# Performance work log

Measured on AMD Instinct MI355X. Metric: run time of the kernel, lower is better.

Reference implementation:

```python
import jax, jax.numpy as jnp
import numpy as np

EPS = 1e-5

def setup_inputs() -> dict:
    key = jax.random.key(0)
    ks = jax.random.split(key, 4)
    n, c, h, w = 4, 256, 64, 64
    attn_chans = 64
    x = jax.random.normal(ks[0], (n, c, h, w), dtype=jnp.float32)
    gamma = jnp.ones((c,), jnp.float32)
    beta = jnp.zeros((c,), jnp.float32)
    qkv_w = jax.random.normal(ks[1], (c, 3 * c), dtype=jnp.float32) / np.sqrt(c)
    proj_w = jax.random.normal(ks[2], (c, c), dtype=jnp.float32) / np.sqrt(c)
    proj_b = jnp.zeros((c,), jnp.float32)
    return {"x": x, "gamma": gamma, "beta": beta, "qkv_w": qkv_w,
            "proj_w": proj_w, "proj_b": proj_b, "attn_chans": attn_chans}


def reference(x, gamma, beta, qkv_w, proj_w, proj_b, attn_chans):
    n, c, h, w = x.shape
    heads = c // attn_chans
    scale = attn_chans ** 0.5
    # BatchNorm2d (training mode: batch statistics, biased variance)
    mean = jnp.mean(x, axis=(0, 2, 3))
    var = jnp.var(x, axis=(0, 2, 3))
    xn = (x - mean[:, None, None]) * jax.lax.rsqrt(var + EPS)[:, None, None]
    xn = xn * gamma[:, None, None] + beta[:, None, None]
    # (n, c, h, w) -> (n, hw, c)
    seq = jnp.transpose(xn.reshape(n, c, h * w), (0, 2, 1))
    qkv = seq @ qkv_w                             # (n, hw, 3c)
    # faithful to torch: view (n, hw, 3c) as (n, heads, hw, 3*attn_chans)
    qkv = qkv.reshape(n, heads, h * w, 3 * attn_chans)
    q, k, v = jnp.split(qkv, 3, axis=-1)          # each (n, heads, hw, d)
    scores = jnp.einsum('nhqd,nhkd->nhqk', q, k) / scale
    attn = jax.nn.softmax(scores, axis=-1)
    o = jnp.einsum('nhqk,nhkd->nhqd', attn, v)    # (n, heads, hw, d)
    o = o.reshape(n, h * w, heads * attn_chans)   # (n, hw, c)
    out = o @ proj_w + proj_b                     # (n, hw, c)
    return jnp.transpose(out, (0, 2, 1)).reshape(n, c, h, w)
```

## Files before the change

kernel.cpp:

```cpp
#include <hip/hip_runtime.h>
#include <stdint.h>

#define NB 4
#define CCH 256
#define HW 4096
#define HEADS 4
#define DH 64
#define SLEN 4096
#define EPSV 1e-5f
#define NEG_INF (-__builtin_inff())
#define QSCALE (0.125f * 1.44269504088896340736f)

typedef unsigned short u16;
typedef __bf16 bf16x8 __attribute__((ext_vector_type(8)));
typedef float f32x4 __attribute__((ext_vector_type(4)));

__device__ __forceinline__ u16 f2bf(float f) {
  union { float f; uint32_t u; } v; v.f = f;
  uint32_t r = v.u + 0x7FFFu + ((v.u >> 16) & 1u);
  return (u16)(r >> 16);
}

__global__ __launch_bounds__(256) void k_pre(
    const float* __restrict__ x, const float* __restrict__ gamma,
    const float* __restrict__ beta, const float* __restrict__ qw,
    const float* __restrict__ pw, float* __restrict__ ab,
    u16* __restrict__ qwb, u16* __restrict__ pwb) {
  int t = threadIdx.x;
  if (blockIdx.x < 256) {
    int ch = blockIdx.x;
    float s = 0.f, ss = 0.f;
    for (int n = 0; n < NB; ++n) {
      const float4* p = (const float4*)(x + ((size_t)(n * CCH + ch)) * HW);
      for (int i = t; i < HW / 4; i += 256) {
        float4 v = p[i];
        s += v.x + v.y + v.z + v.w;
        ss += v.x * v.x + v.y * v.y + v.z * v.z + v.w * v.w;
      }
    }
#pragma unroll
    for (int mm = 32; mm >= 1; mm >>= 1) {
      s += __shfl_down(s, mm);
      ss += __shfl_down(ss, mm);
    }
    __shared__ float ls[4], lss[4];
    if ((t & 63) == 0) { ls[t >> 6] = s; lss[t >> 6] = ss; }
    __syncthreads();
    if (t == 0) {
      float S = 0.f, SS = 0.f;
      for (int i = 0; i < 4; ++i) { S += ls[i]; SS += lss[i]; }
      float inv = 1.0f / (float)(NB * HW);
      float mean = S * inv;
      float var = SS * inv - mean * mean;
      float a = gamma[ch] * rsqrtf(var + EPSV);
      ab[ch] = a;
      ab[CCH + ch] = beta[ch] - mean * a;
    }
  } else {
    const int NQ = CCH * 3 * CCH;
    int i = ((blockIdx.x - 256) * 256 + t) * 8;
    const float* src = (i < NQ) ? (qw + i) : (pw + (i - NQ));
    u16* dst = (i < NQ) ? (qwb + i) : (pwb + (i - NQ));
    float4 v0 = *(const float4*)src;
    float4 v1 = *(const float4*)(src + 4);
    union { u16 u[8]; uint4 v; } o;
    o.u[0] = f2bf(v0.x); o.u[1] = f2bf(v0.y); o.u[2] = f2bf(v0.z); o.u[3] = f2bf(v0.w);
    o.u[4] = f2bf(v1.x); o.u[5] = f2bf(v1.y); o.u[6] = f2bf(v1.z); o.u[7] = f2bf(v1.w);
    *(uint4*)dst = o.v;
  }
}

__global__ __launch_bounds__(256) void k_seq(
    const float* __restrict__ x, const float* __restrict__ ab,
    u16* __restrict__ seq) {
  __shared__ float tile[64][65];
  int pb = blockIdx.x * 64, cb = blockIdx.y * 64, n = blockIdx.z;
  int t = threadIdx.x;
  {
    int cl = t >> 2, pc = (t & 3) * 16;
    float a = ab[cb + cl], b = ab[CCH + cb + cl];
    const float* src = x + ((size_t)(n * CCH + cb + cl)) * HW + pb + pc;
#pragma unroll
    for (int i = 0; i < 4; ++i) {
      float4 v = *(const float4*)(src + i * 4);
      tile[cl][pc + i * 4 + 0] = v.x * a + b;
      tile[cl][pc + i * 4 + 1] = v.y * a + b;
      tile[cl][pc + i * 4 + 2] = v.z * a + b;
      tile[cl][pc + i * 4 + 3] = v.w * a + b;
    }
  }
  __syncthreads();
  {
    int pl = t >> 2, cs = (t & 3) * 16;
    union { u16 u[16]; uint4 v[2]; } tmp;
#pragma unroll
    for (int i = 0; i < 16; ++i) tmp.u[i] = f2bf(tile[cs + i][pl]);
    u16* dst = seq + ((size_t)(n * HW + pb + pl)) * CCH + cb + cs;
    *(uint4*)dst = tmp.v[0];
    *(uint4*)(dst + 8) = tmp.v[1];
  }
}

__global__ __launch_bounds__(256) void k_qkv(
    const u16* __restrict__ seq, const u16* __restrict__ w,
    u16* __restrict__ Q, u16* __restrict__ K, u16* __restrict__ Vt) {
  __shared__ __attribute__((aligned(16))) u16 As[64 * 32];
  __shared__ __attribute__((aligned(16))) u16 Bs[64 * 32];
  int Rb = blockIdx.x * 64, Cb = blockIdx.y * 64;
  int t = threadIdx.x, lane = t & 63, wv = t >> 6;
  int wr = (wv >> 1) * 32, wc = (wv & 1) * 32;
  f32x4 acc[2][2] = {};
  for (int kb = 0; kb < CCH; kb += 32) {
    {
      int r = t >> 2, kc = t & 3;
      uint4 v = *(const uint4*)(seq + ((size_t)(Rb + r)) * CCH + kb + kc * 8);
      *(uint4*)((char*)As + r * 64 + ((kc * 16) ^ ((r & 3) << 4))) = v;
    }
    {
      int k = t >> 3, jc = (t & 7) * 8;
      union { u16 u[8]; uint4 v; } tmp;
      tmp.v = *(const uint4*)(w + ((size_t)(kb + k)) * 768 + Cb + jc);
#pragma unroll
      for (int i2 = 0; i2 < 8; ++i2) {
        int j = jc + i2;
        *(u16*)((char*)Bs + j * 64 + ((k * 2) ^ ((j & 3) << 4))) = tmp.u[i2];
      }
    }
    __syncthreads();
    bf16x8 af[2], bfr[2];
#pragma unroll
    for (int f = 0; f < 2; ++f) {
      int row = wr + f * 16 + (lane & 15);
      af[f] = *(const bf16x8*)((const char*)As + row * 64 +
                               (((lane >> 4) * 16) ^ ((row & 3) << 4)));
      int col = wc + f * 16 + (lane & 15);
      bfr[f] = *(const bf16x8*)((const char*)Bs + col * 64 +
                                (((lane >> 4) * 16) ^ ((col & 3) << 4)));
    }
#pragma unroll
    for (int i2 = 0; i2 < 2; ++i2)
#pragma unroll
      for (int j2 = 0; j2 < 2; ++j2)
        acc[i2][j2] = __builtin_amdgcn_mfma_f32_16x16x32_bf16(af[i2], bfr[j2], acc[i2][j2], 0, 0, 0);
    __syncthreads();
  }
#pragma unroll
  for (int i2 = 0; i2 < 2; ++i2)
#pragma unroll
    for (int j2 = 0; j2 < 2; ++j2)
#pragma unroll
      for (int e = 0; e < 4; ++e) {
        int R = Rb + wr + i2 * 16 + (lane >> 4) * 4 + e;
        int cg = Cb + wc + j2 * 16 + (lane & 15);
        int p = R & (HW - 1);
        int head = p >> 10, mq = p & 1023;
        int qn = mq * 4 + cg / 192, tt = cg % 192;
        int nhx = (R >> 12) * HEADS + head;
        float a = acc[i2][j2][e];
        if (tt < 64)
          Q[((size_t)nhx * SLEN + qn) * DH + tt] = f2bf(a * QSCALE);
        else if (tt < 128)
          K[((size_t)nhx * SLEN + qn) * DH + tt - 64] = f2bf(a);
        else
          Vt[(size_t)nhx * SLEN * DH + (size_t)(tt - 128) * SLEN + qn] = f2bf(a);
      }
}

__global__ __launch_bounds__(256, 2) void k_attn(
    const u16* __restrict__ Q, const u16* __restrict__ K,
    const u16* __restrict__ Vt, u16* __restrict__ O) {
  __shared__ __attribute__((aligned(16))) char smem[32768 + 2048];
  float* mlA = (float*)(smem + 32768);
  float* mlB = (float*)(smem + 32768 + 1024);
  int q0 = blockIdx.x * 64, nh = blockIdx.y;
  int t = threadIdx.x, lane = t & 63, w = t >> 6;
  int l15 = lane & 15, g = lane >> 4;
  size_t base = (size_t)nh * SLEN * DH;
  char* Ps = smem + w * 8192;
  int swz = (l15 & 7) << 4;

  bf16x8 qv[4][2];
#pragma unroll
  for (int qf = 0; qf < 4; ++qf) {
    const u16* qp = Q + base + (size_t)(q0 + qf * 16 + l15) * DH + g * 8;
    qv[qf][0] = *(const bf16x8*)qp;
    qv[qf][1] = *(const bf16x8*)(qp + 32);
  }

  f32x4 o[4][4] = {};
  float m[4] = {NEG_INF, NEG_INF, NEG_INF, NEG_INF};
  float lsum[4] = {0.f, 0.f, 0.f, 0.f};

  const u16* Kbase = K + base + (size_t)l15 * DH + g * 8;
  const u16* Vbase = Vt + base + (size_t)l15 * SLEN + g * 8;

  const int TILES = SLEN / 64 / 4;
  for (int tt = 0; tt < TILES; ++tt) {
    int kv0 = (w * TILES + tt) * 64;
    bf16x8 kf[4][2], vf[4][2];
#pragma unroll
    for (int cf = 0; cf < 4; ++cf) {
      const u16* kp = Kbase + (size_t)(kv0 + cf * 16) * DH;
      kf[cf][0] = *(const bf16x8*)kp;
      kf[cf][1] = *(const bf16x8*)(kp + 32);
    }
#pragma unroll
    for (int df = 0; df < 4; ++df) {
      const u16* vp = Vbase + (size_t)(df * 16) * SLEN + kv0;
      vf[df][0] = *(const bf16x8*)vp;
      vf[df][1] = *(const bf16x8*)(vp + 32);
    }
#pragma unroll
    for (int qf = 0; qf < 4; ++qf) {
      f32x4 st[4];
#pragma unroll
      for (int cf = 0; cf < 4; ++cf) {
        f32x4 a = {};
        a = __builtin_amdgcn_mfma_f32_16x16x32_bf16(kf[cf][0], qv[qf][0], a, 0, 0, 0);
        a = __builtin_amdgcn_mfma_f32_16x16x32_bf16(kf[cf][1], qv[qf][1], a, 0, 0, 0);
        st[cf] = a;
      }
      float mx = st[0][0];
#pragma unroll
      for (int cf = 0; cf < 4; ++cf)
#pragma unroll
        for (int e = 0; e < 4; ++e) mx = fmaxf(mx, st[cf][e]);
      mx = fmaxf(mx, __shfl_xor(mx, 16));
      mx = fmaxf(mx, __shfl_xor(mx, 32));
      if (!__all(mx <= m[qf] + 8.0f)) {
        float mn = fmaxf(m[qf], mx);
        float al = exp2f(m[qf] - mn);
        m[qf] = mn;
        lsum[qf] *= al;
#pragma unroll
        for (int e = 0; e < 4; ++e) {
          float ae = __shfl(al, (lane & 48) | (((lane >> 4) << 2) + e));
#pragma unroll
          for (int df = 0; df < 4; ++df) o[qf][df][e] *= ae;
        }
      }
      float ls = 0.f;
#pragma unroll
      for (int cf = 0; cf < 4; ++cf) {
        union { __bf16 h[4]; uint2 v; } pk;
#pragma unroll
        for (int e = 0; e < 4; ++e) {
          float p = exp2f(st[cf][e] - m[qf]);
          ls += p;
          pk.h[e] = (__bf16)p;
        }
        *(uint2*)(Ps + (qf * 16 + l15) * 128 + ((cf * 32 + g * 8) ^ swz)) = pk.v;
      }
      lsum[qf] += ls;
    }
#pragma unroll
    for (int qf = 0; qf < 4; ++qf) {
#pragma unroll
      for (int ks = 0; ks < 2; ++ks) {
        bf16x8 pa = *(const bf16x8*)(Ps + (qf * 16 + l15) * 128 + ((ks * 64 + g * 16) ^ swz));
#pragma unroll
        for (int df = 0; df < 4; ++df)
          o[qf][df] = __builtin_amdgcn_mfma_f32_16x16x32_bf16(pa, vf[df][ks], o[qf][df], 0, 0, 0);
      }
    }
  }
#pragma unroll
  for (int qf = 0; qf < 4; ++qf) {
    lsum[qf] += __shfl_xor(lsum[qf], 16);
    lsum[qf] += __shfl_xor(lsum[qf], 32);
  }
  f32x4 me[4], le[4];
#pragma unroll
  for (int qf = 0; qf < 4; ++qf)
#pragma unroll
    for (int e = 0; e < 4; ++e) {
      int idx = (lane & 48) | (((lane >> 4) & 3) << 2) | e;
      me[qf][e] = __shfl(m[qf], idx);
      le[qf][e] = __shfl(lsum[qf], idx);
    }

  auto publish = [&](char* reg, int s) {
#pragma unroll
    for (int qf = 0; qf < 4; ++qf) {
#pragma unroll
      for (int df = 0; df < 4; ++df) {
        int d = df * 16 + l15;
        *(f32x4*)(reg + ((d * 256 + qf * 64 + g * 16) ^ ((d & 7) << 4))) = o[qf][df];
      }
      if (l15 == 0) {
        *(f32x4*)&mlA[(s * 4 + qf) * 16 + g * 4] = me[qf];
        *(f32x4*)&mlB[(s * 4 + qf) * 16 + g * 4] = le[qf];
      }
    }
  };
  auto merge = [&](char* reg, int s) {
#pragma unroll
    for (int qf = 0; qf < 4; ++qf) {
      f32x4 mp = *(f32x4*)&mlA[(s * 4 + qf) * 16 + g * 4];
      f32x4 lp = *(f32x4*)&mlB[(s * 4 + qf) * 16 + g * 4];
      f32x4 op[4];
#pragma unroll
      for (int df = 0; df < 4; ++df) {
        int d = df * 16 + l15;
        op[df] = *(f32x4*)(reg + ((d * 256 + qf * 64 + g * 16) ^ ((d & 7) << 4)));
      }
#pragma unroll
      for (int e = 0; e < 4; ++e) {
        float mf = fmaxf(me[qf][e], mp[e]);
        float as = exp2f(me[qf][e] - mf), ap = exp2f(mp[e] - mf);
        le[qf][e] = le[qf][e] * as + lp[e] * ap;
        me[qf][e] = mf;
#pragma unroll
        for (int df = 0; df < 4; ++df)
          o[qf][df][e] = o[qf][df][e] * as + op[df][e] * ap;
      }
    }
  };

  __syncthreads();
  if (w == 1) publish(smem, 1);
  if (w == 3) publish(smem + 16384, 3);
  __syncthreads();
  if (w == 0) merge(smem, 1);
  if (w == 2) merge(smem + 16384, 3);
  __syncthreads();
  if (w == 2) publish(smem, 2);
  __syncthreads();
  if (w == 0) {
    merge(smem, 2);
    int n = nh >> 2, head = nh & 3;
#pragma unroll
    for (int qf = 0; qf < 4; ++qf) {
      f32x4 rinv;
#pragma unroll
      for (int e = 0; e < 4; ++e) rinv[e] = 1.f / le[qf][e];
#pragma unroll
      for (int df = 0; df < 4; ++df) {
        int d = df * 16 + l15;
#pragma unroll
        for (int e = 0; e < 4; ++e) {
          int qn = q0 + qf * 16 + g * 4 + e;
          size_t off = (((size_t)n * HW) + head * 1024 + (qn >> 2)) * CCH + (qn & 3) * DH + d;
          O[off] = f2bf(o[qf][df][e] * rinv[e]);
        }
      }
    }
  }
}

__global__ __launch_bounds__(256) void k_proj(
    const u16* __restrict__ A, const u16* __restrict__ W,
    const float* __restrict__ bias, float* __restrict__ out) {
  __shared__ __attribute__((aligned(16))) u16 As[64 * 32];
  __shared__ __attribute__((aligned(16))) u16 Bs[64 * 32];
  int Rb = blockIdx.x * 64, Cb = blockIdx.y * 64;
  int t = threadIdx.x, lane = t & 63, wv = t >> 6;
  int wr = (wv >> 1) * 32, wc = (wv & 1) * 32;
  f32x4 acc[2][2] = {};
  for (int kb = 0; kb < CCH; kb += 32) {
    {
      int r = t >> 2, kc = t & 3;
      uint4 v = *(const uint4*)(A + ((size_t)(Rb + r)) * CCH + kb + kc * 8);
      *(uint4*)((char*)As + r * 64 + ((kc * 16) ^ ((r & 3) << 4))) = v;
    }
    {
      int k = t >> 3, jc = (t & 7) * 8;
      union { u16 u[8]; uint4 v; } tmp;
      tmp.v = *(const uint4*)(W + ((size_t)(kb + k)) * CCH + Cb + jc);
#pragma unroll
      for (int i2 = 0; i2 < 8; ++i2) {
        int j = jc + i2;
        *(u16*)((char*)Bs + j * 64 + ((k * 2) ^ ((j & 3) << 4))) = tmp.u[i2];
      }
    }
    __syncthreads();
    bf16x8 af[2], bfr[2];
#pragma unroll
    for (int f = 0; f < 2; ++f) {
      int row = wr + f * 16 + (lane & 15);
      af[f] = *(const bf16x8*)((const char*)As + row * 64 +
                               (((lane >> 4) * 16) ^ ((row & 3) << 4)));
      int col = wc + f * 16 + (lane & 15);
      bfr[f] = *(const bf16x8*)((const char*)Bs + col * 64 +
                                (((lane >> 4) * 16) ^ ((col & 3) << 4)));
    }
#pragma unroll
    for (int i2 = 0; i2 < 2; ++i2)
#pragma unroll
      for (int j2 = 0; j2 < 2; ++j2)
        acc[i2][j2] = __builtin_amdgcn_mfma_f32_16x16x32_bf16(af[i2], bfr[j2], acc[i2][j2], 0, 0, 0);
    __syncthreads();
  }
#pragma unroll
  for (int i2 = 0; i2 < 2; ++i2)
#pragma unroll
    for (int j2 = 0; j2 < 2; ++j2)
#pragma unroll
      for (int e = 0; e < 4; ++e) {
        int R = Rb + wr + i2 * 16 + (lane >> 4) * 4 + e;
        int cg = Cb + wc + j2 * 16 + (lane & 15);
        out[((size_t)((R >> 12) * CCH + cg)) * HW + (R & (HW - 1))] =
            acc[i2][j2][e] + bias[cg];
      }
}

extern "C" void kernel_launch(void* const* d_in, const int* in_sizes, int n_in,
                              void* d_out, int out_size, void* d_ws, size_t ws_size,
                              hipStream_t stream) {
  (void)in_sizes; (void)n_in; (void)out_size; (void)ws_size;
  const float* x      = (const float*)d_in[0];
  const float* gamma  = (const float*)d_in[1];
  const float* beta   = (const float*)d_in[2];
  const float* qkv_w  = (const float*)d_in[3];
  const float* proj_w = (const float*)d_in[4];
  const float* proj_b = (const float*)d_in[5];

  char* ws = (char*)d_ws;
  size_t off = 0;
  float* ab = (float*)(ws + off); off += 4096;
  u16* seq  = (u16*)(ws + off);  off += (size_t)NB * HW * CCH * 2;
  u16* qwb  = (u16*)(ws + off);  off += (size_t)CCH * 3 * CCH * 2;
  u16* pwb  = (u16*)(ws + off);  off += (size_t)CCH * CCH * 2;
  u16* Qb   = (u16*)(ws + off);  off += (size_t)NB * HEADS * SLEN * DH * 2;
  u16* Kb   = (u16*)(ws + off);  off += (size_t)NB * HEADS * SLEN * DH * 2;
  u16* Vtb  = (u16*)(ws + off);  off += (size_t)NB * HEADS * SLEN * DH * 2;
  u16* oseq = (u16*)(ws + off);  off += (size_t)NB * HW * CCH * 2;

  k_pre<<<384, 256, 0, stream>>>(x, gamma, beta, qkv_w, proj_w, ab, qwb, pwb);
  k_seq<<<dim3(HW / 64, CCH / 64, NB), 256, 0, stream>>>(x, ab, seq);
  k_qkv<<<dim3((NB * HW) / 64, 768 / 64), 256, 0, stream>>>(seq, qwb, Qb, Kb, Vtb);
  k_attn<<<dim3(SLEN / 64, NB * HEADS), 256, 0, stream>>>(Qb, Kb, Vtb, oseq);
  k_proj<<<dim3((NB * HW) / 64, CCH / 64), 256, 0, stream>>>(oseq, pwb, proj_b, (float*)d_out);
}
```

Measured before the change: 277.2 us.

## Double-buffer K tiles, defer softmax max check, remap attention blocks across XCDs

The attention kernel now prefetches the next K tile into a second register buffer while the current tile's QK and PV run, and loads V just before it is needed. The online-softmax max reduction is skipped unless some exponentiated probability exceeds a threshold, in which case the tile is recomputed with a new max. MFMA sections are wrapped in s_setprio, and the 1D grid is remapped so that consecutive blocks of the same head land on the same XCD for better L2 reuse. The extra register buffer raises register pressure and may reduce occupancy below two blocks per CU.

```diff
diff --git a/kernel.cpp b/kernel.cpp
--- a/kernel.cpp
+++ b/kernel.cpp
@@ -172,7 +172,10 @@
   __shared__ __attribute__((aligned(16))) char smem[32768 + 2048];
   float* mlA = (float*)(smem + 32768);
   float* mlB = (float*)(smem + 32768 + 1024);
-  int q0 = blockIdx.x * 64, nh = blockIdx.y;
+  int bid = blockIdx.x;
+  int wid = (bid & 7) * 128 + (bid >> 3);
+  int nh = wid >> 6;
+  int q0 = (wid & 63) * 64;
   int t = threadIdx.x, lane = t & 63, w = t >> 6;
   int l15 = lane & 15, g = lane >> 4;
   size_t base = (size_t)nh * SLEN * DH;
@@ -191,28 +194,33 @@
   float m[4] = {NEG_INF, NEG_INF, NEG_INF, NEG_INF};
   float lsum[4] = {0.f, 0.f, 0.f, 0.f};
 
-  const u16* Kbase = K + base + (size_t)l15 * DH + g * 8;
-  const u16* Vbase = Vt + base + (size_t)l15 * SLEN + g * 8;
-
-  const int TILES = SLEN / 64 / 4;
-  for (int tt = 0; tt < TILES; ++tt) {
-    int kv0 = (w * TILES + tt) * 64;
-    bf16x8 kf[4][2], vf[4][2];
+  const u16* Kptr = K + base + (size_t)l15 * DH + g * 8;
+  const u16* Vptr = Vt + base + (size_t)l15 * SLEN + g * 8;
+
+  bf16x8 kfA[4][2], kfB[4][2], vf[4][2];
+
+  auto loadK = [&](bf16x8 (&kf)[4][2], int kv0) {
 #pragma unroll
     for (int cf = 0; cf < 4; ++cf) {
-      const u16* kp = Kbase + (size_t)(kv0 + cf * 16) * DH;
+      const u16* kp = Kptr + (size_t)(kv0 + cf * 16) * DH;
       kf[cf][0] = *(const bf16x8*)kp;
       kf[cf][1] = *(const bf16x8*)(kp + 32);
     }
+  };
+  auto loadV = [&](int kv0) {
 #pragma unroll
     for (int df = 0; df < 4; ++df) {
-      const u16* vp = Vbase + (size_t)(df * 16) * SLEN + kv0;
+      const u16* vp = Vptr + (size_t)(df * 16) * SLEN + kv0;
       vf[df][0] = *(const bf16x8*)vp;
       vf[df][1] = *(const bf16x8*)(vp + 32);
     }
+  };
+
+  auto qksoft = [&](bf16x8 (&kf)[4][2]) {
 #pragma unroll
     for (int qf = 0; qf < 4; ++qf) {
       f32x4 st[4];
+      __builtin_amdgcn_s_setprio(1);
 #pragma unroll
       for (int cf = 0; cf < 4; ++cf) {
         f32x4 a = {};
@@ -220,50 +228,89 @@
         a = __builtin_amdgcn_mfma_f32_16x16x32_bf16(kf[cf][1], qv[qf][1], a, 0, 0, 0);
         st[cf] = a;
       }
-      float mx = st[0][0];
-#pragma unroll
-      for (int cf = 0; cf < 4; ++cf)
-#pragma unroll
-        for (int e = 0; e < 4; ++e) mx = fmaxf(mx, st[cf][e]);
-      mx = fmaxf(mx, __shfl_xor(mx, 16));
-      mx = fmaxf(mx, __shfl_xor(mx, 32));
-      if (!__all(mx <= m[qf] + 8.0f)) {
-        float mn = fmaxf(m[qf], mx);
-        float al = exp2f(m[qf] - mn);
-        m[qf] = mn;
-        lsum[qf] *= al;
-#pragma unroll
-        for (int e = 0; e < 4; ++e) {
-          float ae = __shfl(al, (lane & 48) | (((lane >> 4) << 2) + e));
-#pragma unroll
-          for (int df = 0; df < 4; ++df) o[qf][df][e] *= ae;
-        }
-      }
-      float ls = 0.f;
+      __builtin_amdgcn_s_setprio(0);
+      float mq = m[qf];
+      f32x4 lsv = {0.f, 0.f, 0.f, 0.f};
+      f32x4 pmv = {0.f, 0.f, 0.f, 0.f};
 #pragma unroll
       for (int cf = 0; cf < 4; ++cf) {
         union { __bf16 h[4]; uint2 v; } pk;
 #pragma unroll
         for (int e = 0; e < 4; ++e) {
-          float p = exp2f(st[cf][e] - m[qf]);
-          ls += p;
+          float p = exp2f(st[cf][e] - mq);
+          lsv[e] += p;
+          pmv[e] = fmaxf(pmv[e], p);
           pk.h[e] = (__bf16)p;
         }
         *(uint2*)(Ps + (qf * 16 + l15) * 128 + ((cf * 32 + g * 8) ^ swz)) = pk.v;
       }
-      lsum[qf] += ls;
-    }
+      float pmax = fmaxf(fmaxf(pmv[0], pmv[1]), fmaxf(pmv[2], pmv[3]));
+      if (__any(pmax > 256.0f)) {
+        f32x4 mv;
+#pragma unroll
+        for (int e = 0; e < 4; ++e)
+          mv[e] = fmaxf(fmaxf(st[0][e], st[1][e]), fmaxf(st[2][e], st[3][e]));
+        float mx = fmaxf(fmaxf(mv[0], mv[1]), fmaxf(mv[2], mv[3]));
+        mx = fmaxf(mx, __shfl_xor(mx, 16));
+        mx = fmaxf(mx, __shfl_xor(mx, 32));
+        float mn = fmaxf(mq, mx);
+        float al = exp2f(mq - mn);
+        m[qf] = mn;
+        lsum[qf] *= al;
+#pragma unroll
+        for (int e = 0; e < 4; ++e) {
+          float ae = __shfl(al, (lane & 48) | (((lane >> 4) << 2) + e));
+#pragma unroll
+          for (int df = 0; df < 4; ++df) o[qf][df][e] *= ae;
+        }
+        lsv = (f32x4){0.f, 0.f, 0.f, 0.f};
+#pragma unroll
+        for (int cf = 0; cf < 4; ++cf) {
+          union { __bf16 h[4]; uint2 v; } pk;
+#pragma unroll
+          for (int e = 0; e < 4; ++e) {
+            float p = exp2f(st[cf][e] - mn);
+            lsv[e] += p;
+            pk.h[e] = (__bf16)p;
+          }
+          *(uint2*)(Ps + (qf * 16 + l15) * 128 + ((cf * 32 + g * 8) ^ swz)) = pk.v;
+        }
+      }
+      lsum[qf] += lsv[0] + lsv[1] + lsv[2] + lsv[3];
+    }
+  };
+
+  auto pv = [&]() {
 #pragma unroll
     for (int qf = 0; qf < 4; ++qf) {
 #pragma unroll
       for (int ks = 0; ks < 2; ++ks) {
         bf16x8 pa = *(const bf16x8*)(Ps + (qf * 16 + l15) * 128 + ((ks * 64 + g * 16) ^ swz));
+        __builtin_amdgcn_s_setprio(1);
 #pragma unroll
         for (int df = 0; df < 4; ++df)
           o[qf][df] = __builtin_amdgcn_mfma_f32_16x16x32_bf16(pa, vf[df][ks], o[qf][df], 0, 0, 0);
-      }
-    }
-  }
+        __builtin_amdgcn_s_setprio(0);
+      }
+    }
+  };
+
+  const int TILES = SLEN / 64 / 4;
+  int kvBase = w * TILES * 64;
+  loadK(kfA, kvBase);
+  for (int tt = 0; tt < TILES; tt += 2) {
+    int kv0 = kvBase + tt * 64;
+    loadV(kv0);
+    loadK(kfB, kv0 + 64);
+    qksoft(kfA);
+    pv();
+    loadV(kv0 + 64);
+    int nk = (tt + 2 < TILES) ? (kv0 + 128) : kvBase;
+    loadK(kfA, nk);
+    qksoft(kfB);
+    pv();
+  }
+
 #pragma unroll
   for (int qf = 0; qf < 4; ++qf) {
     lsum[qf] += __shfl_xor(lsum[qf], 16);
@@ -429,6 +476,6 @@
   k_pre<<<384, 256, 0, stream>>>(x, gamma, beta, qkv_w, proj_w, ab, qwb, pwb);
   k_seq<<<dim3(HW / 64, CCH / 64, NB), 256, 0, stream>>>(x, ab, seq);
   k_qkv<<<dim3((NB * HW) / 64, 768 / 64), 256, 0, stream>>>(seq, qwb, Qb, Kb, Vtb);
-  k_attn<<<dim3(SLEN / 64, NB * HEADS), 256, 0, stream>>>(Qb, Kb, Vtb, oseq);
+  k_attn<<<1024, 256, 0, stream>>>(Qb, Kb, Vtb, oseq);
   k_proj<<<dim3((NB * HW) / 64, CCH / 64), 256, 0, stream>>>(oseq, pwb, proj_b, (float*)d_out);
 }
```

After: 348.5 us. +25.7%, slower.
